# Performance work log

Hardware: AMD Instinct MI355X
Metric: run time of the kernel (lower is better)

The kernel has to match this reference:

```python
import jax, jax.numpy as jnp
import numpy as np

K = 16
RADIUS = 0.5
LOSS_NORM = 1


def setup_inputs() -> dict:
    key = jax.random.key(0)
    k1, k2 = jax.random.split(key)
    B, N = 2, 8192
    pc = jax.random.normal(k1, (B, N, 3), dtype=jnp.float32)
    flow = jax.random.normal(k2, (B, N, 3), dtype=jnp.float32)
    return {"pc": pc, "flow": flow}


def _ball_query(pc, radius, k):
    """pc: (B,N,3) -> idx (B,N,k) int32. For each query point, the first k
    (in index order) points within radius; empty slots padded with the first
    found index (the query point itself is always in-ball at distance 0),
    matching the pointnet2 CUDA ball_query semantics."""
    B, N, _ = pc.shape
    sq = jnp.sum(pc * pc, axis=-1)  # (B,N)
    # squared pairwise distances via gram matrix: (B,N,N)
    d2 = sq[:, :, None] + sq[:, None, :] - 2.0 * jnp.einsum("bnd,bmd->bnm", pc, pc)
    within = d2 < (radius * radius)
    j = jnp.arange(N, dtype=jnp.int32)
    sentinel = jnp.int32(-2 * N)
    # key = -j for in-ball points, sentinel otherwise; top_k picks smallest j first
    keys = jnp.where(within, -j, sentinel)  # (B,N,N)
    vals, _ = jax.lax.top_k(keys, k)  # (B,N,k)
    idx = -vals
    valid = idx < N
    idx = jnp.where(valid, idx, idx[..., :1])  # pad with first neighbor (self)
    return idx


def reference(pc, flow):
    idx = _ball_query(pc, RADIUS, K)  # (B,N,K)
    # gather neighbor flows: (B,N,K,3)
    nn_flow = jax.vmap(lambda f, i: f[i])(flow, idx)
    diff = flow[:, :, None, :] - nn_flow  # (B,N,K,3)
    if LOSS_NORM == 1:
        norms = jnp.sum(jnp.abs(diff), axis=-1)
    else:
        norms = jnp.sqrt(jnp.sum(diff * diff, axis=-1))
    return jnp.mean(norms)
```

## Files before the change

kernel.cpp:

```cpp
#include <hip/hip_runtime.h>
#include <hip/hip_fp16.h>


#define NQ   8192
#define NB   2
#define KNN  16
#define QPB  64
#define WAVES 8
#define THREADS (QPB * WAVES)
#define NBQ (NB * NQ)
#define GROUPS (NBQ / QPB)
#define SLICES 4
#define SL_PAIRS 1024
#define WPP 128
#define IDXROW 130

static __device__ __forceinline__ unsigned pkrtz_u(float a, float b) {
    return __builtin_bit_cast(unsigned, __builtin_amdgcn_cvt_pkrtz(a, b));
}
static __device__ __forceinline__ __half2 u_as_h2(unsigned u) {
    return __builtin_bit_cast(__half2, u);
}
static __device__ __forceinline__ void bq_pair(unsigned xu, unsigned yu,
                                               unsigned zu, __half2 qpx,
                                               __half2 qpy, __half2 qpz,
                                               __half2 nr2, unsigned& mm) {
    const __half2 dx = __hsub2(qpx, u_as_h2(xu));
    const __half2 dy = __hsub2(qpy, u_as_h2(yu));
    const __half2 dz = __hsub2(qpz, u_as_h2(zu));
    const __half2 t =
        __hfma2(dx, dx, __hfma2(dy, dy, __hfma2(dz, dz, nr2)));
    const unsigned su = __builtin_bit_cast(unsigned, t) & 0x80008000u;
    mm = su | (mm >> 1);
}

__global__ __launch_bounds__(THREADS, 8)
void ballq_scan(const float* __restrict__ pc,
                unsigned short* __restrict__ wsIdx,
                unsigned char* __restrict__ wsCnt)
{
    __shared__ __align__(16) unsigned lx[SL_PAIRS];
    __shared__ __align__(16) unsigned ly[SL_PAIRS];
    __shared__ __align__(16) unsigned lz[SL_PAIRS];
    __shared__ unsigned short s_idx[QPB][IDXROW];
    __shared__ unsigned char  s_cnt[QPB][12];

    const int tid = threadIdx.x;
    const int q   = tid & 63;
    const int c   = tid >> 6;
    const int s   = blockIdx.x & 3;
    const int g   = blockIdx.x >> 2;
    const int b   = g >> 7;
    const int i   = (g & 127) * QPB + q;

    const float* __restrict__ pcb = pc + (size_t)b * NQ * 3;
    const float2* __restrict__ f2 = (const float2*)pcb;

    for (int p = tid; p < SL_PAIRS; p += THREADS) {
        const int gp = s * SL_PAIRS + p;
        const float2 v0 = f2[3 * gp + 0];
        const float2 v1 = f2[3 * gp + 1];
        const float2 v2 = f2[3 * gp + 2];
        lx[p] = pkrtz_u(v0.x, v1.y);
        ly[p] = pkrtz_u(v0.y, v2.x);
        lz[p] = pkrtz_u(v1.x, v2.y);
    }

    const float qx = pcb[i * 3 + 0];
    const float qy = pcb[i * 3 + 1];
    const float qz = pcb[i * 3 + 2];
    const __half2 qpx = u_as_h2(pkrtz_u(qx, qx));
    const __half2 qpy = u_as_h2(pkrtz_u(qy, qy));
    const __half2 qpz = u_as_h2(pkrtz_u(qz, qz));
    const __half2 nr2 = u_as_h2(0xB400B400u);

    __syncthreads();

    int cnt = 0;
    for (int r = 0; r < WPP / 64 && cnt < KNN; ++r) {
        const int pbase = c * WPP + r * 64;
        unsigned m[4] = {0u, 0u, 0u, 0u};
#pragma unroll
        for (int g4 = 0; g4 < 4; ++g4) {
#pragma unroll
            for (int w = 0; w < 4; ++w) {
                const int pb = pbase + w * 16 + g4 * 4;
                const uint4 X = *(const uint4*)&lx[pb];
                const uint4 Y = *(const uint4*)&ly[pb];
                const uint4 Z = *(const uint4*)&lz[pb];
                bq_pair(X.x, Y.x, Z.x, qpx, qpy, qpz, nr2, m[w]);
                bq_pair(X.y, Y.y, Z.y, qpx, qpy, qpz, nr2, m[w]);
                bq_pair(X.z, Y.z, Z.z, qpx, qpy, qpz, nr2, m[w]);
                bq_pair(X.w, Y.w, Z.w, qpx, qpy, qpz, nr2, m[w]);
            }
        }
        unsigned long long ev =
              (unsigned long long)(m[0] & 0xFFFFu)
            | ((unsigned long long)(m[1] & 0xFFFFu) << 16)
            | ((unsigned long long)(m[2] & 0xFFFFu) << 32)
            | ((unsigned long long)(m[3] & 0xFFFFu) << 48);
        unsigned long long od =
              (unsigned long long)(m[0] >> 16)
            | ((unsigned long long)(m[1] >> 16) << 16)
            | ((unsigned long long)(m[2] >> 16) << 32)
            | ((unsigned long long)(m[3] >> 16) << 48);

        const int jb = s * (2 * SL_PAIRS) + 2 * pbase;
        while ((ev | od) && cnt < KNN) {
            const int pe = ev ? __builtin_ctzll(ev) : 127;
            const int po = od ? __builtin_ctzll(od) : 127;
            int j;
            if (pe <= po) { j = jb + 2 * pe;     ev &= ev - 1; }
            else          { j = jb + 2 * po + 1; od &= od - 1; }
            s_idx[q][c * KNN + cnt] = (unsigned short)j;
            ++cnt;
        }
    }
    s_cnt[q][c] = (unsigned char)cnt;
    __syncthreads();

    if (c == 0) {
        const int qid = g * QPB + q;
        unsigned short* __restrict__ rp =
            wsIdx + ((size_t)s * NBQ + qid) * KNN;
        int outc = 0;
        for (int c2 = 0; c2 < WAVES && outc < KNN; ++c2) {
            const int f = s_cnt[q][c2];
            const int take = f < (KNN - outc) ? f : (KNN - outc);
            for (int t = 0; t < take; ++t)
                rp[outc++] = s_idx[q][c2 * KNN + t];
        }
        wsCnt[qid * 4 + s] = (unsigned char)outc;
    }
}

__global__ __launch_bounds__(256)
void ballq_loss(const float* __restrict__ flow,
                const unsigned short* __restrict__ wsIdx,
                const unsigned char* __restrict__ wsCnt,
                float* __restrict__ partial)
{
    const int tid = blockIdx.x * 256 + threadIdx.x;
    const int qid = tid >> 4;
    const int t   = tid & 15;
    const int b   = qid >> 13;
    const int iq  = qid & (NQ - 1);
    const float* __restrict__ flb = flow + (size_t)b * NQ * 3;

    const unsigned cw = *(const unsigned*)(wsCnt + qid * 4);
    const int b0 = cw & 0xFF;
    const int b1 = (cw >> 8)  & 0xFF;
    const int b2 = (cw >> 16) & 0xFF;
    const int c1 = b0, c2c = b0 + b1, c3 = b0 + b1 + b2;
    int tot = c3 + ((cw >> 24) & 0xFF);
    if (tot > KNN) tot = KNN;

    const int seff = (t < tot) ? t : 0;
    const int sl   = (seff >= c1) + (seff >= c2c) + (seff >= c3);
    const int cum  = (sl == 0) ? 0 : (sl == 1) ? c1 : (sl == 2) ? c2c : c3;
    const int j    = wsIdx[((size_t)sl * NBQ + qid) * KNN + (seff - cum)];

    const float fx = flb[iq * 3 + 0];
    const float fy = flb[iq * 3 + 1];
    const float fz = flb[iq * 3 + 2];
    float l = fabsf(fx - flb[j * 3 + 0]) +
              fabsf(fy - flb[j * 3 + 1]) +
              fabsf(fz - flb[j * 3 + 2]);

    for (int o = 32; o > 0; o >>= 1)
        l += __shfl_down(l, o, 64);
    __shared__ float sred[4];
    if ((threadIdx.x & 63) == 0) sred[threadIdx.x >> 6] = l;
    __syncthreads();
    if (threadIdx.x == 0)
        partial[blockIdx.x] = sred[0] + sred[1] + sred[2] + sred[3];
}

__global__ __launch_bounds__(1024)
void ballq_final(const float* __restrict__ partial, float* __restrict__ out)
{
    const int tid = threadIdx.x;
    float v = partial[tid];
    for (int o = 32; o > 0; o >>= 1)
        v += __shfl_down(v, o, 64);
    __shared__ float s[16];
    if ((tid & 63) == 0) s[tid >> 6] = v;
    __syncthreads();
    if (tid == 0) {
        float t = 0.0f;
#pragma unroll
        for (int w = 0; w < 16; ++w) t += s[w];
        out[0] = t * (1.0f / ((float)NB * NQ * KNN));
    }
}

extern "C" void kernel_launch(void* const* d_in, const int* in_sizes, int n_in,
                              void* d_out, int out_size, void* d_ws, size_t ws_size,
                              hipStream_t stream)
{
    (void)in_sizes; (void)n_in; (void)out_size; (void)ws_size;
    const float* pc   = (const float*)d_in[0];
    const float* flow = (const float*)d_in[1];
    float* out = (float*)d_out;

    unsigned short* wsIdx = (unsigned short*)d_ws;
    unsigned char*  wsCnt = (unsigned char*)d_ws + (size_t)SLICES * NBQ * KNN * 2;
    float* partial = (float*)(wsCnt + (size_t)NBQ * 4);

    ballq_scan<<<GROUPS * SLICES, THREADS, 0, stream>>>(pc, wsIdx, wsCnt);
    ballq_loss<<<NBQ * 16 / 256, 256, 0, stream>>>(flow, wsIdx, wsCnt, partial);
    ballq_final<<<1, 1024, 0, stream>>>(partial, out);
}
```

Before: 36.84 us.

## Pre-pack half2 point coordinates in a prep kernel and read them via scalar loads

Adds a prep kernel that converts the point cloud once into packed half2 SoA arrays in workspace. The scan kernel drops its per-block LDS staging loop and the barrier after it. It now reads candidate coordinates straight from global memory with wave-uniform addresses (readfirstlane on the wave index), which lets them become scalar or broadcast loads. This removes the repeated fp32-to-half conversion and the LDS traffic, at the cost of one extra kernel launch and global or scalar-cache reads inside the inner loop.

Measured after the change: 40.97 us. 1.11x slower.

```diff
diff --git a/kernel.cpp b/kernel.cpp
--- a/kernel.cpp
+++ b/kernel.cpp
@@ -13,6 +13,7 @@
 #define SLICES 4
 #define SL_PAIRS 1024
 #define WPP 128
+#define NPAIRS (NQ / 2)
 #define IDXROW 130
 
 static __device__ __forceinline__ unsigned pkrtz_u(float a, float b) {
@@ -34,38 +35,39 @@
     mm = su | (mm >> 1);
 }
 
+__global__ __launch_bounds__(256)
+void ballq_prep(const float* __restrict__ pc, unsigned* __restrict__ wsPk)
+{
+    const int p  = blockIdx.x * 256 + threadIdx.x;
+    const int b  = p >> 12;
+    const int pp = p & (NPAIRS - 1);
+    const float2* __restrict__ f2 = (const float2*)(pc + (size_t)b * NQ * 3);
+    const float2 v0 = f2[3 * pp + 0];
+    const float2 v1 = f2[3 * pp + 1];
+    const float2 v2 = f2[3 * pp + 2];
+    wsPk[(b * 3 + 0) * NPAIRS + pp] = pkrtz_u(v0.x, v1.y);
+    wsPk[(b * 3 + 1) * NPAIRS + pp] = pkrtz_u(v0.y, v2.x);
+    wsPk[(b * 3 + 2) * NPAIRS + pp] = pkrtz_u(v1.x, v2.y);
+}
+
 __global__ __launch_bounds__(THREADS, 8)
 void ballq_scan(const float* __restrict__ pc,
+                const unsigned* __restrict__ wsPk,
                 unsigned short* __restrict__ wsIdx,
                 unsigned char* __restrict__ wsCnt)
 {
-    __shared__ __align__(16) unsigned lx[SL_PAIRS];
-    __shared__ __align__(16) unsigned ly[SL_PAIRS];
-    __shared__ __align__(16) unsigned lz[SL_PAIRS];
     __shared__ unsigned short s_idx[QPB][IDXROW];
     __shared__ unsigned char  s_cnt[QPB][12];
 
     const int tid = threadIdx.x;
     const int q   = tid & 63;
-    const int c   = tid >> 6;
+    const int cU  = __builtin_amdgcn_readfirstlane(tid >> 6);
     const int s   = blockIdx.x & 3;
     const int g   = blockIdx.x >> 2;
     const int b   = g >> 7;
     const int i   = (g & 127) * QPB + q;
 
     const float* __restrict__ pcb = pc + (size_t)b * NQ * 3;
-    const float2* __restrict__ f2 = (const float2*)pcb;
-
-    for (int p = tid; p < SL_PAIRS; p += THREADS) {
-        const int gp = s * SL_PAIRS + p;
-        const float2 v0 = f2[3 * gp + 0];
-        const float2 v1 = f2[3 * gp + 1];
-        const float2 v2 = f2[3 * gp + 2];
-        lx[p] = pkrtz_u(v0.x, v1.y);
-        ly[p] = pkrtz_u(v0.y, v2.x);
-        lz[p] = pkrtz_u(v1.x, v2.y);
-    }
-
     const float qx = pcb[i * 3 + 0];
     const float qy = pcb[i * 3 + 1];
     const float qz = pcb[i * 3 + 2];
@@ -74,20 +76,23 @@
     const __half2 qpz = u_as_h2(pkrtz_u(qz, qz));
     const __half2 nr2 = u_as_h2(0xB400B400u);
 
-    __syncthreads();
+    const uint4* __restrict__ px4 = (const uint4*)(wsPk + (b * 3 + 0) * NPAIRS);
+    const uint4* __restrict__ py4 = (const uint4*)(wsPk + (b * 3 + 1) * NPAIRS);
+    const uint4* __restrict__ pz4 = (const uint4*)(wsPk + (b * 3 + 2) * NPAIRS);
 
     int cnt = 0;
     for (int r = 0; r < WPP / 64 && cnt < KNN; ++r) {
-        const int pbase = c * WPP + r * 64;
+        const int pbase = s * SL_PAIRS + cU * WPP + r * 64;
+        const int q4    = pbase >> 2;
         unsigned m[4] = {0u, 0u, 0u, 0u};
 #pragma unroll
         for (int g4 = 0; g4 < 4; ++g4) {
 #pragma unroll
             for (int w = 0; w < 4; ++w) {
-                const int pb = pbase + w * 16 + g4 * 4;
-                const uint4 X = *(const uint4*)&lx[pb];
-                const uint4 Y = *(const uint4*)&ly[pb];
-                const uint4 Z = *(const uint4*)&lz[pb];
+                const int u4 = q4 + w * 4 + g4;
+                const uint4 X = px4[u4];
+                const uint4 Y = py4[u4];
+                const uint4 Z = pz4[u4];
                 bq_pair(X.x, Y.x, Z.x, qpx, qpy, qpz, nr2, m[w]);
                 bq_pair(X.y, Y.y, Z.y, qpx, qpy, qpz, nr2, m[w]);
                 bq_pair(X.z, Y.z, Z.z, qpx, qpy, qpz, nr2, m[w]);
@@ -105,21 +110,21 @@
             | ((unsigned long long)(m[2] >> 16) << 32)
             | ((unsigned long long)(m[3] >> 16) << 48);
 
-        const int jb = s * (2 * SL_PAIRS) + 2 * pbase;
+        const int jb = 2 * pbase;
         while ((ev | od) && cnt < KNN) {
             const int pe = ev ? __builtin_ctzll(ev) : 127;
             const int po = od ? __builtin_ctzll(od) : 127;
             int j;
             if (pe <= po) { j = jb + 2 * pe;     ev &= ev - 1; }
             else          { j = jb + 2 * po + 1; od &= od - 1; }
-            s_idx[q][c * KNN + cnt] = (unsigned short)j;
+            s_idx[q][cU * KNN + cnt] = (unsigned short)j;
             ++cnt;
         }
     }
-    s_cnt[q][c] = (unsigned char)cnt;
+    s_cnt[q][cU] = (unsigned char)cnt;
     __syncthreads();
 
-    if (c == 0) {
+    if (cU == 0) {
         const int qid = g * QPB + q;
         unsigned short* __restrict__ rp =
             wsIdx + ((size_t)s * NBQ + qid) * KNN;
@@ -203,11 +208,13 @@
     const float* flow = (const float*)d_in[1];
     float* out = (float*)d_out;
 
-    unsigned short* wsIdx = (unsigned short*)d_ws;
-    unsigned char*  wsCnt = (unsigned char*)d_ws + (size_t)SLICES * NBQ * KNN * 2;
+    unsigned*       wsPk  = (unsigned*)d_ws;
+    unsigned short* wsIdx = (unsigned short*)((char*)d_ws + (size_t)NB * 3 * NPAIRS * 4);
+    unsigned char*  wsCnt = (unsigned char*)wsIdx + (size_t)SLICES * NBQ * KNN * 2;
     float* partial = (float*)(wsCnt + (size_t)NBQ * 4);
 
-    ballq_scan<<<GROUPS * SLICES, THREADS, 0, stream>>>(pc, wsIdx, wsCnt);
+    ballq_prep<<<NB * NPAIRS / 256, 256, 0, stream>>>(pc, wsPk);
+    ballq_scan<<<GROUPS * SLICES, THREADS, 0, stream>>>(pc, wsPk, wsIdx, wsCnt);
     ballq_loss<<<NBQ * 16 / 256, 256, 0, stream>>>(flow, wsIdx, wsCnt, partial);
     ballq_final<<<1, 1024, 0, stream>>>(partial, out);
 }
```
